# Optimization experiments

Hardware: AMD Instinct MI355X
Metric: run time of the kernel (lower is better)

## Reference

```python
import jax, jax.numpy as jnp
import numpy as np

COND_SIZE = 512
LR_SCALE = 1.0 / np.sqrt(COND_SIZE)  # equalized-lr scale for the style linear
EPS = 1e-8


def _style(condition, w):
    # lr_equal(nn.Linear(cond_size, in_size, bias=False)): runtime weight scale 1/sqrt(fan_in)
    return (condition @ w.T) * LR_SCALE  # [B, Cin]


def _mod_demod_conv(x, w, b, style):
    # x [B,Cin,H,W], w [Cout,Cin,3,3], style [B,Cin]
    wmod = w[None] * style[:, None, :, None, None]               # [B,Cout,Cin,3,3]
    demod = jax.lax.rsqrt(jnp.sum(wmod * wmod, axis=(2, 3, 4)) + EPS)  # [B,Cout]
    wmod = wmod * demod[:, :, None, None, None]
    conv1 = lambda xi, wi: jax.lax.conv_general_dilated(
        xi[None], wi, window_strides=(1, 1), padding='SAME')[0]
    out = jax.vmap(conv1)(x, wmod)                                # per-sample weights
    return out + b[None, :, None, None]


def setup_inputs() -> dict:
    key = jax.random.key(0)
    ks = jax.random.split(key, 12)
    B, Cin, Cout, H, W = 8, 128, 64, 256, 256
    return {
        'inputs': jax.random.normal(ks[0], (B, Cin, H, W), jnp.float32),
        'condition': jax.random.normal(ks[1], (B, COND_SIZE), jnp.float32),
        'cond_w0': jax.random.normal(ks[2], (Cin, COND_SIZE), jnp.float32),
        'cond_w1': jax.random.normal(ks[3], (Cin, COND_SIZE), jnp.float32),
        'conv_w0': jax.random.normal(ks[4], (Cin, Cin, 3, 3), jnp.float32) * 0.05,
        'conv_b0': jnp.zeros((Cin,), jnp.float32),
        'conv_w1': jax.random.normal(ks[5], (Cout, Cin, 3, 3), jnp.float32) * 0.05,
        'conv_b1': jnp.zeros((Cout,), jnp.float32),
        'noise_scale0': jax.random.normal(ks[6], (Cin,), jnp.float32),
        'noise_scale1': jax.random.normal(ks[7], (Cout,), jnp.float32),
        'noise0': jax.random.normal(ks[8], (B, Cin, H, W), jnp.float32),
        'noise1': jax.random.normal(ks[9], (B, Cout, H, W), jnp.float32),
        'rgb_w': jax.random.normal(ks[10], (3, Cout), jnp.float32) * 0.05,
        'rgb_b': jnp.zeros((3,), jnp.float32),
    }


def reference(inputs, condition, cond_w0, cond_w1, conv_w0, conv_b0,
              conv_w1, conv_b1, noise_scale0, noise_scale1,
              noise0, noise1, rgb_w, rgb_b):
    # block 0: modulated/demodulated 3x3 conv + channel-scaled noise injection
    out = _mod_demod_conv(inputs, conv_w0, conv_b0, _style(condition, cond_w0))
    out = out + noise0 * noise_scale0[None, :, None, None]
    # block 1
    out = _mod_demod_conv(out, conv_w1, conv_b1, _style(condition, cond_w1))
    out = out + noise1 * noise_scale1[None, :, None, None]
    # 1x1 to-RGB conv
    rgb = jnp.einsum('bchw,oc->bohw', out, rgb_w) + rgb_b[None, :, None, None]
    return (out, rgb)
```

## Files before the change

### kernel.cpp

```cpp
#include <hip/hip_runtime.h>
#include <stdint.h>
#include <stddef.h>


typedef __bf16 bf16;
typedef __bf16 bf16x8 __attribute__((ext_vector_type(8)));
typedef float  f32x4  __attribute__((ext_vector_type(4)));

#define AS1 __attribute__((address_space(1)))
#define AS3 __attribute__((address_space(3)))

#define OFF_A1    0ull
#define OFF_WT0   134217728ull
#define OFF_WT1   134512640ull
#define OFF_S0    134660096ull
#define OFF_S1    134664192ull
#define OFF_DM0   134668288ull
#define OFF_DM1   134672384ull
#define OFF_WSQ0  134674432ull
#define OFF_WSQ1  134739968ull
#define OFF_ZP    134772736ull

static __device__ __forceinline__ void gload_lds16(const void* src, void* ldsdst) {
  __builtin_amdgcn_global_load_lds((const AS1 void*)src, (AS3 void*)ldsdst, 16, 0, 0);
}

__global__ __launch_bounds__(256) void k_prep1(
    const float* __restrict__ cond, const float* __restrict__ cw0,
    const float* __restrict__ cw1, const float* __restrict__ w0,
    const float* __restrict__ w1, float* __restrict__ s0, float* __restrict__ s1,
    bf16* __restrict__ wt0, bf16* __restrict__ wt1,
    float* __restrict__ wsq0, float* __restrict__ wsq1, float* __restrict__ zp)
{
  int idx = blockIdx.x * 256 + threadIdx.x;
  if (idx < 2048) {
    int which = idx >> 10; int b = (idx >> 7) & 7; int c = idx & 127;
    const float* cw = which ? cw1 : cw0;
    const float* cp = cond + b * 512;
    const float* wp = cw + c * 512;
    float acc = 0.f;
    for (int j = 0; j < 512; ++j) acc += cp[j] * wp[j];
    (which ? s1 : s0)[b * 128 + c] = acc * 0.044194173824159216f;
    return;
  }
  idx -= 2048;
  if (idx < 147456) {
    int t = idx >> 14;
    wt0[idx] = (bf16)w0[(idx & 16383) * 9 + t];
    return;
  }
  idx -= 147456;
  if (idx < 73728) {
    int t = idx >> 13;
    wt1[idx] = (bf16)w1[(idx & 8191) * 9 + t];
    return;
  }
  idx -= 73728;
  if (idx < 16384) {
    const float* p = w0 + idx * 9; float a = 0.f;
    #pragma unroll
    for (int t = 0; t < 9; ++t) a += p[t] * p[t];
    wsq0[idx] = a; return;
  }
  idx -= 16384;
  if (idx < 8192) {
    const float* p = w1 + idx * 9; float a = 0.f;
    #pragma unroll
    for (int t = 0; t < 9; ++t) a += p[t] * p[t];
    wsq1[idx] = a; return;
  }
  idx -= 8192;
  if (idx < 64) zp[idx] = 0.f;
}

__global__ __launch_bounds__(256) void k_prep2(
    const float* __restrict__ s0, const float* __restrict__ s1,
    const float* __restrict__ wsq0, const float* __restrict__ wsq1,
    float* __restrict__ dm0, float* __restrict__ dm1)
{
  int idx = blockIdx.x * 256 + threadIdx.x;
  if (idx < 1024) {
    int b = idx >> 7, co = idx & 127;
    const float* sp = s0 + b * 128; const float* wp = wsq0 + co * 128;
    float a = 0.f;
    for (int ci = 0; ci < 128; ++ci) { float s = sp[ci]; a += s * s * wp[ci]; }
    dm0[idx] = rsqrtf(a + 1e-8f);
  } else if (idx < 1536) {
    int j = idx - 1024; int b = j >> 6, co = j & 63;
    const float* sp = s1 + b * 128; const float* wp = wsq1 + co * 128;
    float a = 0.f;
    for (int ci = 0; ci < 128; ++ci) { float s = sp[ci]; a += s * s * wp[ci]; }
    dm1[j] = rsqrtf(a + 1e-8f);
  }
}

__global__ __launch_bounds__(256) void k_mod(
    const float* __restrict__ x, const float* __restrict__ s0, bf16* __restrict__ A0)
{
  __shared__ alignas(16) char lds[8192];
  int bid = blockIdx.x;
  int b = bid >> 11; int rem = bid & 2047; int h = rem >> 3; int wp0 = (rem & 7) << 5;
  int t = threadIdx.x;
  #pragma unroll
  for (int iter = 0; iter < 2; ++iter) {
    int idx = iter * 256 + t; int w = idx & 31; int chunk = idx >> 5;
    const float* xp = x + (((size_t)(b * 128 + chunk * 8)) << 16) + (h << 8) + wp0 + w;
    const float* sp = s0 + b * 128 + chunk * 8;
    bf16x8 v;
    #pragma unroll
    for (int i = 0; i < 8; ++i) v[i] = (bf16)(xp[(size_t)i << 16] * sp[i]);
    *(bf16x8*)(lds + w * 256 + ((chunk ^ (w & 7)) << 4)) = v;
  }
  __syncthreads();
  #pragma unroll
  for (int iter = 0; iter < 2; ++iter) {
    int idx = iter * 256 + t; int w = idx >> 4; int c = idx & 15;
    bf16x8 v = *(const bf16x8*)(lds + w * 256 + ((c ^ (w & 7)) << 4));
    *(bf16x8*)(A0 + ((((size_t)(b << 16)) + (h << 8) + wp0 + w) << 7) + (c << 3)) = v;
  }
}

constexpr int cDY[9] = {0,0,0,1,1,1,2,2,2};
constexpr int cDX[9] = {0,1,2,0,1,2,0,1,2};

static __device__ __forceinline__ void stage_tileA(
    const bf16* __restrict__ src, const bf16* __restrict__ zp, char* Abase,
    int b, int h0, int w0p, int wave, int lane)
{
  #pragma unroll
  for (int i = 0; i < 12; ++i) {
    int g = wave + (i << 2);
    if (g < 45) {
      int pin = (g << 2) + (lane >> 4); int j = lane & 15;
      int r = pin / 18; int c = pin - r * 18;
      int gh = h0 - 1 + r, gw = w0p - 1 + c;
      const bf16* s;
      if (((unsigned)gh < 256u) & ((unsigned)gw < 256u))
        s = src + ((((size_t)(b << 16)) + (gh << 8) + gw) << 7) + ((j ^ (pin & 7)) << 3);
      else
        s = zp;
      gload_lds16(s, Abase + (size_t)g * 1024);
    }
  }
}

__global__ __launch_bounds__(256, 2) void k_conv0(
    const bf16* __restrict__ A0, const bf16* __restrict__ wt,
    const float* __restrict__ dm, const float* __restrict__ bias,
    const float* __restrict__ noise, const float* __restrict__ nsc,
    const float* __restrict__ s1, const bf16* __restrict__ zp,
    bf16* __restrict__ A1)
{
  extern __shared__ __align__(16) char lds[];
  char* Abase = lds;
  char* Bp0 = lds + 46080;
  char* Bp1 = lds + 54272;
  char* Bp2 = lds + 62464;

  int bid = blockIdx.x;
  int wg = (bid & 7) * 512 + (bid >> 3);
  int b = wg >> 9; int rem = wg & 511;
  int h0 = (rem >> 4) << 3; int w0p = (rem & 15) << 4;
  int tid = threadIdx.x; int wave = tid >> 6; int lane = tid & 63;

  auto stageB = [&](int s, char* dst) {
    const int t = s >> 2, ci = (s & 3) << 5;
    #pragma unroll
    for (int i = 0; i < 2; ++i) {
      int co_base = (wave << 4) + (i << 6);
      int co = co_base + (lane >> 2);
      int kgs = (lane & 3) ^ ((co >> 1) & 3);
      gload_lds16(wt + ((size_t)t << 14) + co * 128 + ci + (kgs << 3),
                  dst + co_base * 64);
    }
  };

  stage_tileA(A0, zp, Abase, b, h0, w0p, wave, lane);
  stageB(0, Bp0);
  stageB(1, Bp1);
  asm volatile("s_waitcnt vmcnt(2)" ::: "memory");
  __builtin_amdgcn_s_barrier();

  int m16 = lane & 15, kg = lane >> 4;
  int pb = (wave >> 1) << 6, cb = (wave & 1) << 6;
  int basePin[4];
  #pragma unroll
  for (int mr = 0; mr < 4; ++mr)
    basePin[mr] = ((pb >> 4) + mr) * 18 + m16;

  f32x4 acc[4][4] = {};
  #pragma unroll
  for (int s = 0; s < 36; ++s) {
    char* Bcur = (s % 3 == 0) ? Bp0 : ((s % 3 == 1) ? Bp1 : Bp2);
    const int t = s >> 2, c4 = s & 3;
    const int dy = cDY[t], dx = cDX[t];
    bf16x8 a[4], bwv[4];
    #pragma unroll
    for (int mr = 0; mr < 4; ++mr) {
      int pin = basePin[mr] + dy * 18 + dx;
      int cc = (c4 << 2) + kg;
      a[mr] = *(const bf16x8*)(Abase + pin * 256 + ((cc ^ (pin & 7)) << 4));
    }
    #pragma unroll
    for (int nr = 0; nr < 4; ++nr) {
      int co = cb + nr * 16 + m16;
      int slot = kg ^ ((co >> 1) & 3);
      bwv[nr] = *(const bf16x8*)(Bcur + co * 64 + (slot << 4));
    }
    if (s + 2 < 36) {
      const int sn = s + 2;
      char* Bnxt = (sn % 3 == 0) ? Bp0 : ((sn % 3 == 1) ? Bp1 : Bp2);
      stageB(sn, Bnxt);
    }
    __builtin_amdgcn_s_setprio(1);
    #pragma unroll
    for (int mr = 0; mr < 4; ++mr)
      #pragma unroll
      for (int nr = 0; nr < 4; ++nr)
        acc[mr][nr] = __builtin_amdgcn_mfma_f32_16x16x32_bf16(
            a[mr], bwv[nr], acc[mr][nr], 0, 0, 0);
    __builtin_amdgcn_s_setprio(0);
    if (s <= 33) {
      asm volatile("s_waitcnt vmcnt(2)" ::: "memory");
      __builtin_amdgcn_s_barrier();
    } else if (s == 34) {
      asm volatile("s_waitcnt vmcnt(0)" ::: "memory");
      __builtin_amdgcn_s_barrier();
    }
  }
  __syncthreads();

  float* zl = (float*)lds;
  #pragma unroll
  for (int half = 0; half < 2; ++half) {
    if ((wave >> 1) == half) {
      #pragma unroll
      for (int nr = 0; nr < 4; ++nr) {
        int co = cb + nr * 16 + m16;
        float d = dm[(b << 7) + co], bb = bias[co];
        #pragma unroll
        for (int mr = 0; mr < 4; ++mr) {
          int p0 = mr * 16 + (kg << 2);
          #pragma unroll
          for (int r = 0; r < 4; ++r)
            zl[(p0 + r) * 129 + co] = acc[mr][nr][r] * d + bb;
        }
      }
    }
    __syncthreads();
    #pragma unroll 4
    for (int it = 0; it < 32; ++it) {
      int idx = it * 256 + tid; int co = idx >> 6; int p6 = idx & 63;
      int gh = h0 + (half << 2) + (p6 >> 4), gw = w0p + (p6 & 15);
      float n = noise[(((size_t)((b << 7) + co)) << 16) + (gh << 8) + gw];
      float y = zl[p6 * 129 + co] + n * nsc[co];
      zl[p6 * 129 + co] = y * s1[(b << 7) + co];
    }
    __syncthreads();
    #pragma unroll
    for (int it = 0; it < 4; ++it) {
      int idx = it * 256 + tid; int p6 = idx >> 4; int ch = idx & 15;
      int gh = h0 + (half << 2) + (p6 >> 4), gw = w0p + (p6 & 15);
      const float* zpt = zl + p6 * 129 + (ch << 3);
      bf16x8 v;
      #pragma unroll
      for (int i = 0; i < 8; ++i) v[i] = (bf16)zpt[i];
      *(bf16x8*)(A1 + ((((size_t)(b << 16)) + (gh << 8) + gw) << 7) + (ch << 3)) = v;
    }
    __syncthreads();
  }
}

__global__ __launch_bounds__(256, 2) void k_conv1(
    const bf16* __restrict__ A1, const bf16* __restrict__ wt,
    const float* __restrict__ dm, const float* __restrict__ bias,
    const float* __restrict__ noise, const float* __restrict__ nsc,
    const float* __restrict__ rgbw, const float* __restrict__ rgbb,
    const bf16* __restrict__ zp, float* __restrict__ out, float* __restrict__ rgb)
{
  __shared__ alignas(16) char lds[58368];
  char* Abase = lds;
  char* Bp0 = lds + 46080;
  char* Bp1 = lds + 50176;
  char* Bp2 = lds + 54272;

  int bid = blockIdx.x;
  int wg = (bid & 7) * 512 + (bid >> 3);
  int b = wg >> 9; int rem = wg & 511;
  int h0 = (rem >> 4) << 3; int w0p = (rem & 15) << 4;
  int tid = threadIdx.x; int wave = tid >> 6; int lane = tid & 63;

  auto stageB = [&](int s, char* dst) {
    const int t = s >> 2, ci = (s & 3) << 5;
    int co_base = wave << 4;
    int co = co_base + (lane >> 2);
    int kgs = (lane & 3) ^ ((co >> 1) & 3);
    gload_lds16(wt + ((size_t)t << 13) + co * 128 + ci + (kgs << 3),
                dst + co_base * 64);
  };

  stage_tileA(A1, zp, Abase, b, h0, w0p, wave, lane);
  stageB(0, Bp0);
  stageB(1, Bp1);
  asm volatile("s_waitcnt vmcnt(1)" ::: "memory");
  __builtin_amdgcn_s_barrier();

  int m16 = lane & 15, kg = lane >> 4;
  int pb = (wave >> 1) << 6, cb = (wave & 1) << 5;
  int basePin[4];
  #pragma unroll
  for (int mr = 0; mr < 4; ++mr)
    basePin[mr] = ((pb >> 4) + mr) * 18 + m16;

  f32x4 acc[4][2] = {};
  #pragma unroll
  for (int s = 0; s < 36; ++s) {
    char* Bcur = (s % 3 == 0) ? Bp0 : ((s % 3 == 1) ? Bp1 : Bp2);
    const int t = s >> 2, c4 = s & 3;
    const int dy = cDY[t], dx = cDX[t];
    bf16x8 a[4], bwv[2];
    #pragma unroll
    for (int mr = 0; mr < 4; ++mr) {
      int pin = basePin[mr] + dy * 18 + dx;
      int cc = (c4 << 2) + kg;
      a[mr] = *(const bf16x8*)(Abase + pin * 256 + ((cc ^ (pin & 7)) << 4));
    }
    #pragma unroll
    for (int nr = 0; nr < 2; ++nr) {
      int co = cb + nr * 16 + m16;
      int slot = kg ^ ((co >> 1) & 3);
      bwv[nr] = *(const bf16x8*)(Bcur + co * 64 + (slot << 4));
    }
    if (s + 2 < 36) {
      const int sn = s + 2;
      char* Bnxt = (sn % 3 == 0) ? Bp0 : ((sn % 3 == 1) ? Bp1 : Bp2);
      stageB(sn, Bnxt);
    }
    __builtin_amdgcn_s_setprio(1);
    #pragma unroll
    for (int mr = 0; mr < 4; ++mr)
      #pragma unroll
      for (int nr = 0; nr < 2; ++nr)
        acc[mr][nr] = __builtin_amdgcn_mfma_f32_16x16x32_bf16(
            a[mr], bwv[nr], acc[mr][nr], 0, 0, 0);
    __builtin_amdgcn_s_setprio(0);
    if (s <= 33) {
      asm volatile("s_waitcnt vmcnt(1)" ::: "memory");
      __builtin_amdgcn_s_barrier();
    } else if (s == 34) {
      asm volatile("s_waitcnt vmcnt(0)" ::: "memory");
      __builtin_amdgcn_s_barrier();
    }
  }
  __syncthreads();

  float* zl = (float*)lds;
  #pragma unroll
  for (int nr = 0; nr < 2; ++nr) {
    int co = cb + nr * 16 + m16;
    float d = dm[(b << 6) + co], bb = bias[co];
    #pragma unroll
    for (int mr = 0; mr < 4; ++mr) {
      int p0 = pb + mr * 16 + (kg << 2);
      #pragma unroll
      for (int r = 0; r < 4; ++r)
        zl[(p0 + r) * 65 + co] = acc[mr][nr][r] * d + bb;
    }
  }
  __syncthreads();
  #pragma unroll 4
  for (int it = 0; it < 32; ++it) {
    int idx = it * 256 + tid; int co = idx >> 7; int p = idx & 127;
    int gh = h0 + (p >> 4), gw = w0p + (p & 15);
    size_t go = (((size_t)((b << 6) + co)) << 16) + (gh << 8) + gw;
    float y = zl[p * 65 + co] + noise[go] * nsc[co];
    zl[p * 65 + co] = y;
    out[go] = y;
  }
  __syncthreads();
  if (tid < 128) {
    int p = tid; int gh = h0 + (p >> 4), gw = w0p + (p & 15);
    float r0 = rgbb[0], r1 = rgbb[1], r2 = rgbb[2];
    for (int co = 0; co < 64; ++co) {
      float v = zl[p * 65 + co];
      r0 += v * rgbw[co]; r1 += v * rgbw[64 + co]; r2 += v * rgbw[128 + co];
    }
    size_t base = (((size_t)(b * 3)) << 16) + (gh << 8) + gw;
    rgb[base] = r0; rgb[base + (1 << 16)] = r1; rgb[base + (2 << 16)] = r2;
  }
}

extern "C" void kernel_launch(void* const* d_in, const int* in_sizes, int n_in,
                              void* d_out, int out_size, void* d_ws, size_t ws_size,
                              hipStream_t stream)
{
  const float* x      = (const float*)d_in[0];
  const float* cond   = (const float*)d_in[1];
  const float* cw0    = (const float*)d_in[2];
  const float* cw1    = (const float*)d_in[3];
  const float* w0     = (const float*)d_in[4];
  const float* b0     = (const float*)d_in[5];
  const float* w1     = (const float*)d_in[6];
  const float* b1     = (const float*)d_in[7];
  const float* ns0    = (const float*)d_in[8];
  const float* ns1    = (const float*)d_in[9];
  const float* noise0 = (const float*)d_in[10];
  const float* noise1 = (const float*)d_in[11];
  const float* rgbw   = (const float*)d_in[12];
  const float* rgbb   = (const float*)d_in[13];

  char* ws = (char*)d_ws;
  bf16*  A1   = (bf16*)(ws + OFF_A1);
  bf16*  WT0  = (bf16*)(ws + OFF_WT0);
  bf16*  WT1  = (bf16*)(ws + OFF_WT1);
  float* S0   = (float*)(ws + OFF_S0);
  float* S1   = (float*)(ws + OFF_S1);
  float* DM0  = (float*)(ws + OFF_DM0);
  float* DM1  = (float*)(ws + OFF_DM1);
  float* WSQ0 = (float*)(ws + OFF_WSQ0);
  float* WSQ1 = (float*)(ws + OFF_WSQ1);
  float* ZP   = (float*)(ws + OFF_ZP);

  float* out = (float*)d_out;
  float* rgb = out + 33554432;

  bf16* A0 = (bf16*)d_out;

  hipFuncSetAttribute((const void*)k_conv0,
                      hipFuncAttributeMaxDynamicSharedMemorySize, 70656);

  k_prep1<<<dim3(969), dim3(256), 0, stream>>>(cond, cw0, cw1, w0, w1,
                                               S0, S1, WT0, WT1, WSQ0, WSQ1, ZP);
  k_prep2<<<dim3(6), dim3(256), 0, stream>>>(S0, S1, WSQ0, WSQ1, DM0, DM1);
  k_mod<<<dim3(16384), dim3(256), 0, stream>>>(x, S0, A0);
  k_conv0<<<dim3(4096), dim3(256), 70656, stream>>>(A0, WT0, DM0, b0, noise0, ns0,
                                                    S1, (const bf16*)ZP, A1);
  k_conv1<<<dim3(4096), dim3(256), 0, stream>>>(A1, WT1, DM1, b1, noise1, ns1,
                                                rgbw, rgbb, (const bf16*)ZP, out, rgb);
}
```

Before: 478.4 us.

## Stage conv input tile in two channel halves to shrink LDS and raise occupancy

Both conv kernels now load the 18x10 input halo tile one 64-channel half at a time instead of all 128 channels at once. This roughly halves the A-tile LDS footprint. Launch bounds rise to 3 blocks per CU for conv0 and 4 for conv1, and conv0 drops dynamic shared memory for a static array. The K loop is reordered so the first 18 steps use the first channel half. At step 17 the kernel fully drains memory, barriers and reloads the second half, which adds a pipeline bubble in exchange for more resident blocks to hide latency.

After: 665.9 us. +39.2%, slower.

```diff
diff --git a/kernel.cpp b/kernel.cpp
--- a/kernel.cpp
+++ b/kernel.cpp
@@ -123,20 +123,21 @@
 constexpr int cDY[9] = {0,0,0,1,1,1,2,2,2};
 constexpr int cDX[9] = {0,1,2,0,1,2,0,1,2};
 
-static __device__ __forceinline__ void stage_tileA(
+static __device__ __forceinline__ void stage_tileA_half(
     const bf16* __restrict__ src, const bf16* __restrict__ zp, char* Abase,
-    int b, int h0, int w0p, int wave, int lane)
-{
-  #pragma unroll
-  for (int i = 0; i < 12; ++i) {
+    int b, int h0, int w0p, int half, int wave, int lane)
+{
+  #pragma unroll
+  for (int i = 0; i < 6; ++i) {
     int g = wave + (i << 2);
-    if (g < 45) {
-      int pin = (g << 2) + (lane >> 4); int j = lane & 15;
+    if (g < 23) {
+      int pin = (g << 3) + (lane >> 3); int j = lane & 7;
       int r = pin / 18; int c = pin - r * 18;
       int gh = h0 - 1 + r, gw = w0p - 1 + c;
       const bf16* s;
-      if (((unsigned)gh < 256u) & ((unsigned)gw < 256u))
-        s = src + ((((size_t)(b << 16)) + (gh << 8) + gw) << 7) + ((j ^ (pin & 7)) << 3);
+      if ((pin < 180) & ((unsigned)gh < 256u) & ((unsigned)gw < 256u))
+        s = src + ((((size_t)(b << 16)) + (gh << 8) + gw) << 7) + (half << 6)
+              + ((j ^ (pin & 7)) << 3);
       else
         s = zp;
       gload_lds16(s, Abase + (size_t)g * 1024);
@@ -144,18 +145,18 @@
   }
 }
 
-__global__ __launch_bounds__(256, 2) void k_conv0(
+__global__ __launch_bounds__(256, 3) void k_conv0(
     const bf16* __restrict__ A0, const bf16* __restrict__ wt,
     const float* __restrict__ dm, const float* __restrict__ bias,
     const float* __restrict__ noise, const float* __restrict__ nsc,
     const float* __restrict__ s1, const bf16* __restrict__ zp,
     bf16* __restrict__ A1)
 {
-  extern __shared__ __align__(16) char lds[];
+  __shared__ alignas(16) char lds[48128];
   char* Abase = lds;
-  char* Bp0 = lds + 46080;
-  char* Bp1 = lds + 54272;
-  char* Bp2 = lds + 62464;
+  char* Bp0 = lds + 23552;
+  char* Bp1 = lds + 31744;
+  char* Bp2 = lds + 39936;
 
   int bid = blockIdx.x;
   int wg = (bid & 7) * 512 + (bid >> 3);
@@ -164,18 +165,20 @@
   int tid = threadIdx.x; int wave = tid >> 6; int lane = tid & 63;
 
   auto stageB = [&](int s, char* dst) {
-    const int t = s >> 2, ci = (s & 3) << 5;
+    const int hh = (s >= 18) ? 1 : 0;
+    const int sl = s - 18 * hh;
+    const int t = sl >> 1, c4h = sl & 1;
     #pragma unroll
     for (int i = 0; i < 2; ++i) {
       int co_base = (wave << 4) + (i << 6);
       int co = co_base + (lane >> 2);
       int kgs = (lane & 3) ^ ((co >> 1) & 3);
-      gload_lds16(wt + ((size_t)t << 14) + co * 128 + ci + (kgs << 3),
+      gload_lds16(wt + ((size_t)t << 14) + co * 128 + (hh << 6) + (c4h << 5) + (kgs << 3),
                   dst + co_base * 64);
     }
   };
 
-  stage_tileA(A0, zp, Abase, b, h0, w0p, wave, lane);
+  stage_tileA_half(A0, zp, Abase, b, h0, w0p, 0, wave, lane);
   stageB(0, Bp0);
   stageB(1, Bp1);
   asm volatile("s_waitcnt vmcnt(2)" ::: "memory");
@@ -192,14 +195,16 @@
   #pragma unroll
   for (int s = 0; s < 36; ++s) {
     char* Bcur = (s % 3 == 0) ? Bp0 : ((s % 3 == 1) ? Bp1 : Bp2);
-    const int t = s >> 2, c4 = s & 3;
+    const int hh = (s >= 18) ? 1 : 0;
+    const int sl = s - 18 * hh;
+    const int t = sl >> 1, c4h = sl & 1;
     const int dy = cDY[t], dx = cDX[t];
     bf16x8 a[4], bwv[4];
     #pragma unroll
     for (int mr = 0; mr < 4; ++mr) {
       int pin = basePin[mr] + dy * 18 + dx;
-      int cc = (c4 << 2) + kg;
-      a[mr] = *(const bf16x8*)(Abase + pin * 256 + ((cc ^ (pin & 7)) << 4));
+      int cc = (c4h << 2) + kg;
+      a[mr] = *(const bf16x8*)(Abase + pin * 128 + ((cc ^ (pin & 7)) << 4));
     }
     #pragma unroll
     for (int nr = 0; nr < 4; ++nr) {
@@ -220,7 +225,13 @@
         acc[mr][nr] = __builtin_amdgcn_mfma_f32_16x16x32_bf16(
             a[mr], bwv[nr], acc[mr][nr], 0, 0, 0);
     __builtin_amdgcn_s_setprio(0);
-    if (s <= 33) {
+    if (s == 17) {
+      asm volatile("s_waitcnt vmcnt(2)" ::: "memory");
+      __builtin_amdgcn_s_barrier();
+      stage_tileA_half(A0, zp, Abase, b, h0, w0p, 1, wave, lane);
+      asm volatile("s_waitcnt vmcnt(0)" ::: "memory");
+      __builtin_amdgcn_s_barrier();
+    } else if (s <= 33) {
       asm volatile("s_waitcnt vmcnt(2)" ::: "memory");
       __builtin_amdgcn_s_barrier();
     } else if (s == 34) {
@@ -271,18 +282,18 @@
   }
 }
 
-__global__ __launch_bounds__(256, 2) void k_conv1(
+__global__ __launch_bounds__(256, 4) void k_conv1(
     const bf16* __restrict__ A1, const bf16* __restrict__ wt,
     const float* __restrict__ dm, const float* __restrict__ bias,
     const float* __restrict__ noise, const float* __restrict__ nsc,
     const float* __restrict__ rgbw, const float* __restrict__ rgbb,
     const bf16* __restrict__ zp, float* __restrict__ out, float* __restrict__ rgb)
 {
-  __shared__ alignas(16) char lds[58368];
+  __shared__ alignas(16) char lds[35840];
   char* Abase = lds;
-  char* Bp0 = lds + 46080;
-  char* Bp1 = lds + 50176;
-  char* Bp2 = lds + 54272;
+  char* Bp0 = lds + 23552;
+  char* Bp1 = lds + 27648;
+  char* Bp2 = lds + 31744;
 
   int bid = blockIdx.x;
   int wg = (bid & 7) * 512 + (bid >> 3);
@@ -291,15 +302,17 @@
   int tid = threadIdx.x; int wave = tid >> 6; int lane = tid & 63;
 
   auto stageB = [&](int s, char* dst) {
-    const int t = s >> 2, ci = (s & 3) << 5;
+    const int hh = (s >= 18) ? 1 : 0;
+    const int sl = s - 18 * hh;
+    const int t = sl >> 1, c4h = sl & 1;
     int co_base = wave << 4;
     int co = co_base + (lane >> 2);
     int kgs = (lane & 3) ^ ((co >> 1) & 3);
-    gload_lds16(wt + ((size_t)t << 13) + co * 128 + ci + (kgs << 3),
+    gload_lds16(wt + ((size_t)t << 13) + co * 128 + (hh << 6) + (c4h << 5) + (kgs << 3),
                 dst + co_base * 64);
   };
 
-  stage_tileA(A1, zp, Abase, b, h0, w0p, wave, lane);
+  stage_tileA_half(A1, zp, Abase, b, h0, w0p, 0, wave, lane);
   stageB(0, Bp0);
   stageB(1, Bp1);
   asm volatile("s_waitcnt vmcnt(1)" ::: "memory");
@@ -316,14 +329,16 @@
   #pragma unroll
   for (int s = 0; s < 36; ++s) {
     char* Bcur = (s % 3 == 0) ? Bp0 : ((s % 3 == 1) ? Bp1 : Bp2);
-    const int t = s >> 2, c4 = s & 3;
+    const int hh = (s >= 18) ? 1 : 0;
+    const int sl = s - 18 * hh;
+    const int t = sl >> 1, c4h = sl & 1;
     const int dy = cDY[t], dx = cDX[t];
     bf16x8 a[4], bwv[2];
     #pragma unroll
     for (int mr = 0; mr < 4; ++mr) {
       int pin = basePin[mr] + dy * 18 + dx;
-      int cc = (c4 << 2) + kg;
-      a[mr] = *(const bf16x8*)(Abase + pin * 256 + ((cc ^ (pin & 7)) << 4));
+      int cc = (c4h << 2) + kg;
+      a[mr] = *(const bf16x8*)(Abase + pin * 128 + ((cc ^ (pin & 7)) << 4));
     }
     #pragma unroll
     for (int nr = 0; nr < 2; ++nr) {
@@ -344,7 +359,13 @@
         acc[mr][nr] = __builtin_amdgcn_mfma_f32_16x16x32_bf16(
             a[mr], bwv[nr], acc[mr][nr], 0, 0, 0);
     __builtin_amdgcn_s_setprio(0);
-    if (s <= 33) {
+    if (s == 17) {
+      asm volatile("s_waitcnt vmcnt(1)" ::: "memory");
+      __builtin_amdgcn_s_barrier();
+      stage_tileA_half(A1, zp, Abase, b, h0, w0p, 1, wave, lane);
+      asm volatile("s_waitcnt vmcnt(0)" ::: "memory");
+      __builtin_amdgcn_s_barrier();
+    } else if (s <= 33) {
       asm volatile("s_waitcnt vmcnt(1)" ::: "memory");
       __builtin_amdgcn_s_barrier();
     } else if (s == 34) {
@@ -426,15 +447,12 @@
 
   bf16* A0 = (bf16*)d_out;
 
-  hipFuncSetAttribute((const void*)k_conv0,
-                      hipFuncAttributeMaxDynamicSharedMemorySize, 70656);
-
   k_prep1<<<dim3(969), dim3(256), 0, stream>>>(cond, cw0, cw1, w0, w1,
                                                S0, S1, WT0, WT1, WSQ0, WSQ1, ZP);
   k_prep2<<<dim3(6), dim3(256), 0, stream>>>(S0, S1, WSQ0, WSQ1, DM0, DM1);
   k_mod<<<dim3(16384), dim3(256), 0, stream>>>(x, S0, A0);
-  k_conv0<<<dim3(4096), dim3(256), 70656, stream>>>(A0, WT0, DM0, b0, noise0, ns0,
-                                                    S1, (const bf16*)ZP, A1);
+  k_conv0<<<dim3(4096), dim3(256), 0, stream>>>(A0, WT0, DM0, b0, noise0, ns0,
+                                                S1, (const bf16*)ZP, A1);
   k_conv1<<<dim3(4096), dim3(256), 0, stream>>>(A1, WT1, DM1, b1, noise1, ns1,
                                                 rgbw, rgbb, (const bf16*)ZP, out, rgb);
 }
```
